# Optimization experiments

Hardware: AMD Instinct MI355X
Metric: run time of the kernel (lower is better)

Reference implementation:

```python
import jax, jax.numpy as jnp
import numpy as np


def _l2norm(t, axis=-1, eps=1e-12):
    # matches torch F.normalize: x / max(||x||, eps)
    n = jnp.sqrt(jnp.sum(t * t, axis=axis, keepdims=True))
    return t / jnp.maximum(n, eps)


def setup_inputs() -> dict:
    key = jax.random.key(0)
    ks = jax.random.split(key, 5)
    B, N, C, H = 16, 4096, 768, 12
    x = jax.random.normal(ks[0], (B, N, C), dtype=jnp.float32)
    Wqkv = jax.random.normal(ks[1], (C, 3 * C), dtype=jnp.float32) * (C ** -0.5)
    bqkv = jax.random.normal(ks[2], (3 * C,), dtype=jnp.float32) * 0.02
    Wproj = jax.random.normal(ks[3], (C, C), dtype=jnp.float32) * (C ** -0.5)
    bproj = jax.random.normal(ks[4], (C,), dtype=jnp.float32) * 0.02
    temperature = jnp.ones((H, 1, 1), dtype=jnp.float32)
    return {"x": x, "Wqkv": Wqkv, "bqkv": bqkv, "Wproj": Wproj,
            "bproj": bproj, "temperature": temperature}


def reference(x, Wqkv, bqkv, Wproj, bproj, temperature):
    B, N, C = x.shape
    H = temperature.shape[0]
    Dh = C // H
    qkv = x @ Wqkv + bqkv                      # [B,N,3C]
    qkv = qkv.reshape(B, N, 3, H, Dh)
    # -> [3,B,H,Dh,N] (channels-as-tokens layout)
    qkv = jnp.transpose(qkv, (2, 0, 3, 4, 1))
    q, k, v = qkv[0], qkv[1], qkv[2]           # each [B,H,Dh,N]
    q = _l2norm(q, axis=-1)
    k = _l2norm(k, axis=-1)
    # cross-covariance over channels: [B,H,Dh,Dh]
    attn = jnp.einsum('bhdn,bhen->bhde', q, k) * temperature
    attn = jax.nn.softmax(attn, axis=-1)
    out = jnp.einsum('bhde,bhen->bhdn', attn, v)  # [B,H,Dh,N]
    out = jnp.transpose(out, (0, 3, 1, 2)).reshape(B, N, C)
    return out @ Wproj + bproj
```

## Files before the change

### kernel.cpp

```cpp
#include <hip/hip_runtime.h>

typedef __bf16 bf16x8 __attribute__((ext_vector_type(8)));
typedef float  f32x4  __attribute__((ext_vector_type(4)));
typedef unsigned short u16x8 __attribute__((ext_vector_type(8)));
typedef unsigned short u16x4 __attribute__((ext_vector_type(4)));

#define MFMA16(a, b, c) __builtin_amdgcn_mfma_f32_16x16x32_bf16((a), (b), (c), 0, 0, 0)

#define GLOAD16(g, l) __builtin_amdgcn_global_load_lds( \
    (const __attribute__((address_space(1))) void*)(g),  \
    (__attribute__((address_space(3))) void*)(l), 16, 0, 0)

__device__ __forceinline__ float bf2f(unsigned short u) {
    unsigned int x = ((unsigned int)u) << 16;
    return __builtin_bit_cast(float, x);
}
__device__ __forceinline__ unsigned short f2bf(float f) {
    unsigned int x = __builtin_bit_cast(unsigned int, f);
    x = x + 0x7FFFu + ((x >> 16) & 1u);
    return (unsigned short)(x >> 16);
}
__device__ __forceinline__ bool is_f32(const unsigned short* tf) { return tf[0] == 0; }
__device__ __forceinline__ float ldscal(const void* p, int i, bool f32m) {
    return f32m ? ((const float*)p)[i] : bf2f(((const unsigned short*)p)[i]);
}

__global__ __launch_bounds__(256)
void conv_x(const void* __restrict__ in, unsigned short* __restrict__ out,
            const unsigned short* __restrict__ tf)
{
    const bool f32m = is_f32(tf);
    const int n8 = 6291456;
    for (int i = blockIdx.x * 256 + threadIdx.x; i < n8; i += gridDim.x * 256) {
        u16x8 v;
        if (f32m) {
            const float* p = (const float*)in + (size_t)i * 8;
            f32x4 a = *(const f32x4*)p;
            f32x4 b = *(const f32x4*)(p + 4);
#pragma unroll
            for (int j = 0; j < 4; ++j) { v[j] = f2bf(a[j]); v[4 + j] = f2bf(b[j]); }
        } else {
            v = *(const u16x8*)((const unsigned short*)in + (size_t)i * 8);
        }
        *(u16x8*)&out[(size_t)i * 8] = v;
    }
}

__global__ __launch_bounds__(256)
void tr_conv(const void* __restrict__ in_, unsigned short* __restrict__ out,
             int R, int C, int istride, const unsigned short* __restrict__ tf)
{
    __shared__ unsigned short T[64 * 72];
    const bool f32m = is_f32(tf);
    const int nct = C >> 6;
    const int tx = blockIdx.x % nct;
    const int ty = blockIdx.x / nct;
    const int r0 = ty * 64, c0 = tx * 64;
    const int t = threadIdx.x;
#pragma unroll
    for (int s = 0; s < 2; ++s) {
        const int idx = t + s * 256;
        const int rr = idx >> 3;
        const int cc = (idx & 7) * 8;
        unsigned short v[8];
        if (f32m) {
            const float* inf = (const float*)in_;
            f32x4 a = *(const f32x4*)&inf[(size_t)(r0 + rr) * istride + c0 + cc];
            f32x4 b = *(const f32x4*)&inf[(size_t)(r0 + rr) * istride + c0 + cc + 4];
#pragma unroll
            for (int j = 0; j < 4; ++j) { v[j] = f2bf(a[j]); v[4 + j] = f2bf(b[j]); }
        } else {
            u16x8 a = *(const u16x8*)&((const unsigned short*)in_)[(size_t)(r0 + rr) * istride + c0 + cc];
#pragma unroll
            for (int j = 0; j < 8; ++j) v[j] = a[j];
        }
#pragma unroll
        for (int j = 0; j < 8; ++j) T[(cc + j) * 72 + rr] = v[j];
    }
    __syncthreads();
#pragma unroll
    for (int s = 0; s < 2; ++s) {
        const int idx = t + s * 256;
        const int cc = idx >> 3;
        const int rr = (idx & 7) * 8;
        u16x8 v = *(const u16x8*)&T[cc * 72 + rr];
        *(u16x8*)&out[(size_t)(c0 + cc) * R + r0 + rr] = v;
    }
}

__global__ __launch_bounds__(256)
void conv_wv(const void* __restrict__ Wqkv, unsigned short* __restrict__ Wv_bf,
             const unsigned short* __restrict__ tf)
{
    const bool f32m = is_f32(tf);
    const int t = blockIdx.x * 256 + threadIdx.x;
    const int c = t / 96;
    const int e0 = (t % 96) * 8;
    u16x8 v;
    if (f32m) {
        const float* p = (const float*)Wqkv + (size_t)c * 2304 + 1536 + e0;
        f32x4 a = *(const f32x4*)p;
        f32x4 b = *(const f32x4*)(p + 4);
#pragma unroll
        for (int j = 0; j < 4; ++j) { v[j] = f2bf(a[j]); v[4 + j] = f2bf(b[j]); }
    } else {
        v = *(const u16x8*)&((const unsigned short*)Wqkv)[(size_t)c * 2304 + 1536 + e0];
    }
    *(u16x8*)&Wv_bf[(size_t)c * 768 + e0] = v;
}

template<int MODE>
__global__ __launch_bounds__(512, 2)
void gemm256(const unsigned short* __restrict__ A,
             const unsigned short* __restrict__ BT,
             const void* __restrict__ bias,
             unsigned short* __restrict__ o0,
             unsigned short* __restrict__ o1,
             float* __restrict__ oF,
             const unsigned short* __restrict__ tf)
{
    constexpr int K = 768, NT = 12;
    constexpr int NB = (MODE == 0) ? 6 : 3;
    constexpr int LDSSZ = (MODE == 0) ? 135168 : 131072;
    __shared__ __align__(16) char SM[LDSSZ];
    unsigned short* lds = (unsigned short*)SM;

    const bool f32m = is_f32(tf);
    const int tid  = threadIdx.x;
    const int wave = tid >> 6;
    const int lane = tid & 63;
    const int wm   = wave >> 2;
    const int wn   = wave & 3;
    const int lr   = lane & 15;
    const int lq   = lane >> 4;

    const int per = gridDim.x >> 3;
    const int wg  = (blockIdx.x & 7) * per + (blockIdx.x >> 3);
    const int mt  = wg / NB;
    const int nt  = wg % NB;
    const size_t m0 = (size_t)mt * 256;
    const int n0 = nt * 256;

    const unsigned short* Bt = BT + ((MODE == 1) ? ((m0 >> 12) * (size_t)589824) : (size_t)0);

    f32x4 zero = {0.f, 0.f, 0.f, 0.f};
    f32x4 acc[8][4];
#pragma unroll
    for (int i = 0; i < 8; ++i)
#pragma unroll
        for (int j = 0; j < 4; ++j) acc[i][j] = zero;

    auto STAGE = [&](int t) {
        unsigned short* la = lds + (t & 1) * 32768;
        unsigned short* lb = la + 16384;
        const unsigned short* ga = A  + m0 * K + t * 64;
        const unsigned short* gb = Bt + (size_t)n0 * K + t * 64;
#pragma unroll
        for (int it = 0; it < 4; ++it) {
            const int c = it * 512 + tid;
            const int row = c >> 3;
            const int gs = (c & 7) ^ (row & 7);
            GLOAD16(ga + (size_t)row * K + gs * 8, la + c * 8);
        }
#pragma unroll
        for (int it = 0; it < 4; ++it) {
            const int c = it * 512 + tid;
            const int row = c >> 3;
            const int gs = (c & 7) ^ (row & 7);
            GLOAD16(gb + (size_t)row * K + gs * 8, lb + c * 8);
        }
    };

    STAGE(0);
    STAGE(1);

    for (int t = 0; t < NT; ++t) {
        if (t + 1 < NT) asm volatile("s_waitcnt vmcnt(8)" ::: "memory");
        else            asm volatile("s_waitcnt vmcnt(0)" ::: "memory");
        __builtin_amdgcn_s_barrier();
        __builtin_amdgcn_sched_barrier(0);

        const char* la = (const char*)(lds + (t & 1) * 32768);
        const char* lb = la + 32768;

        bf16x8 bfr[4][2];
#pragma unroll
        for (int ni = 0; ni < 4; ++ni)
#pragma unroll
            for (int ks = 0; ks < 2; ++ks) {
                const int row = wn * 64 + ni * 16 + lr;
                const int s   = ks * 4 + lq;
                bfr[ni][ks] = *(const bf16x8*)(lb + row * 128 + ((s ^ (row & 7)) << 4));
            }
#pragma unroll
        for (int mh = 0; mh < 2; ++mh) {
            bf16x8 af[4][2];
#pragma unroll
            for (int mi = 0; mi < 4; ++mi)
#pragma unroll
                for (int ks = 0; ks < 2; ++ks) {
                    const int row = wm * 128 + mh * 64 + mi * 16 + lr;
                    const int s   = ks * 4 + lq;
                    af[mi][ks] = *(const bf16x8*)(la + row * 128 + ((s ^ (row & 7)) << 4));
                }
            __builtin_amdgcn_s_setprio(1);
#pragma unroll
            for (int mi = 0; mi < 4; ++mi)
#pragma unroll
                for (int ni = 0; ni < 4; ++ni)
#pragma unroll
                    for (int ks = 0; ks < 2; ++ks)
                        acc[mh * 4 + mi][ni] = MFMA16(af[mi][ks], bfr[ni][ks], acc[mh * 4 + mi][ni]);
            __builtin_amdgcn_s_setprio(0);
        }

        __builtin_amdgcn_sched_barrier(0);
        __builtin_amdgcn_s_barrier();
        if (t + 2 < NT) STAGE(t + 2);
    }

    float bb[4];
#pragma unroll
    for (int ni = 0; ni < 4; ++ni) {
        const int col = n0 + wn * 64 + ni * 16 + lr;
        if (MODE == 0)      bb[ni] = ldscal(bias, col, f32m);
        else if (MODE == 1) bb[ni] = ((const float*)bias)[(m0 >> 12) * 768 + col];
        else                bb[ni] = 0.f;
    }

    if (MODE == 1 || MODE == 2) {
#pragma unroll
        for (int mi = 0; mi < 8; ++mi)
#pragma unroll
            for (int ni = 0; ni < 4; ++ni)
#pragma unroll
                for (int r = 0; r < 4; ++r) {
                    const size_t row = m0 + (size_t)(wm * 128 + mi * 16 + lq * 4 + r);
                    const int col = n0 + wn * 64 + ni * 16 + lr;
                    const float val = acc[mi][ni][r] + bb[ni];
                    if (MODE == 2)      o0[row * 768 + col] = f2bf(val);
                    else if (f32m)      oF[row * 768 + col] = val;
                    else                o0[row * 768 + col] = f2bf(val);
                }
    } else {
        unsigned short* CTw = (unsigned short*)SM + wave * (64 * 132);
        const int cbase = (n0 < 768) ? n0 : (n0 - 768);
        unsigned short* dst = (n0 < 768) ? o0 : o1;
        const int h = (cbase >> 6) + wn;
        const size_t bh = (m0 >> 12) * 12 + h;
        const int tokbase = (int)(m0 & 4095) + wm * 128;
#pragma unroll
        for (int mi = 0; mi < 8; ++mi)
#pragma unroll
            for (int ni = 0; ni < 4; ++ni) {
                u16x4 pk;
#pragma unroll
                for (int r = 0; r < 4; ++r) pk[r] = f2bf(acc[mi][ni][r] + bb[ni]);
                *(u16x4*)&CTw[(ni * 16 + lr) * 132 + mi * 16 + lq * 4] = pk;
            }
#pragma unroll
        for (int rep = 0; rep < 16; ++rep) {
            const int d = rep * 4 + lq;
            u16x8 v = *(const u16x8*)&CTw[d * 132 + lr * 8];
            *(u16x8*)&dst[(bh * 64 + d) * 4096 + tokbase + lr * 8] = v;
        }
    }
}

__global__ __launch_bounds__(256)
void attn_sm(const unsigned short* __restrict__ qt,
             const unsigned short* __restrict__ ktb,
             const unsigned short* __restrict__ tf,
             unsigned short* __restrict__ attnT)
{
    __shared__ float S[64][64];
    __shared__ float nq[64];
    __shared__ float nk[64];
    const bool f32m = is_f32(tf);
    const int bh = blockIdx.x;
    const int h = bh % 12;
    const unsigned short* Q  = qt  + (size_t)bh * (64 * 4096);
    const unsigned short* Kp = ktb + (size_t)bh * (64 * 4096);
    const int tid = threadIdx.x;
    const int wave = tid >> 6;
    const int lane = tid & 63;
    if (tid < 64) { nq[tid] = 0.f; nk[tid] = 0.f; }

    f32x4 zero = {0.f, 0.f, 0.f, 0.f};
    f32x4 acc[4][4];
#pragma unroll
    for (int i = 0; i < 4; ++i)
#pragma unroll
        for (int j = 0; j < 4; ++j) acc[i][j] = zero;
    float sq[4] = {0.f, 0.f, 0.f, 0.f};
    float sk[4] = {0.f, 0.f, 0.f, 0.f};

    const int lr = lane & 15;
    const int lk = (lane >> 4) * 8;

    for (int it = 0; it < 32; ++it) {
        const int nb = (it * 4 + wave) * 32 + lk;
        u16x8 qa[4], ka[4];
#pragma unroll
        for (int mi = 0; mi < 4; ++mi)
            qa[mi] = *(const u16x8*)&Q[(size_t)(mi * 16 + lr) * 4096 + nb];
#pragma unroll
        for (int ni = 0; ni < 4; ++ni)
            ka[ni] = *(const u16x8*)&Kp[(size_t)(ni * 16 + lr) * 4096 + nb];
#pragma unroll
        for (int mi = 0; mi < 4; ++mi)
#pragma unroll
            for (int j = 0; j < 8; ++j) { float f = bf2f(qa[mi][j]); sq[mi] += f * f; }
#pragma unroll
        for (int ni = 0; ni < 4; ++ni)
#pragma unroll
            for (int j = 0; j < 8; ++j) { float f = bf2f(ka[ni][j]); sk[ni] += f * f; }
#pragma unroll
        for (int mi = 0; mi < 4; ++mi)
#pragma unroll
            for (int ni = 0; ni < 4; ++ni)
                acc[mi][ni] = MFMA16(__builtin_bit_cast(bf16x8, qa[mi]),
                                     __builtin_bit_cast(bf16x8, ka[ni]),
                                     acc[mi][ni]);
    }

    for (int ww = 0; ww < 4; ++ww) {
        if (wave == ww) {
#pragma unroll
            for (int mi = 0; mi < 4; ++mi)
#pragma unroll
                for (int ni = 0; ni < 4; ++ni)
#pragma unroll
                    for (int r = 0; r < 4; ++r) {
                        const int d = mi * 16 + (lane >> 4) * 4 + r;
                        const int e = ni * 16 + lr;
                        if (ww == 0) S[d][e] = acc[mi][ni][r];
                        else         S[d][e] += acc[mi][ni][r];
                    }
        }
        __syncthreads();
    }

#pragma unroll
    for (int mi = 0; mi < 4; ++mi) {
        float v = sq[mi];
        v += __shfl_xor(v, 16); v += __shfl_xor(v, 32);
        if (lane < 16) atomicAdd(&nq[mi * 16 + lane], v);
        float v2 = sk[mi];
        v2 += __shfl_xor(v2, 16); v2 += __shfl_xor(v2, 32);
        if (lane < 16) atomicAdd(&nk[mi * 16 + lane], v2);
    }
    __syncthreads();

    const int d  = tid >> 2;
    const int qq = tid & 3;
    const float tv = f32m ? ((const float*)tf)[h] : bf2f(tf[h]);
    const float qn = fmaxf(sqrtf(nq[d]), 1e-12f);
    float vals[16];
    float mx = -1e30f;
#pragma unroll
    for (int i = 0; i < 16; ++i) {
        const int e = qq * 16 + i;
        const float s = S[d][e] / (qn * fmaxf(sqrtf(nk[e]), 1e-12f)) * tv;
        vals[i] = s;
        mx = fmaxf(mx, s);
    }
    mx = fmaxf(mx, __shfl_xor(mx, 1));
    mx = fmaxf(mx, __shfl_xor(mx, 2));
    float sum = 0.f;
#pragma unroll
    for (int i = 0; i < 16; ++i) { vals[i] = __expf(vals[i] - mx); sum += vals[i]; }
    sum += __shfl_xor(sum, 1);
    sum += __shfl_xor(sum, 2);
    const float inv = 1.0f / sum;
#pragma unroll
    for (int i = 0; i < 16; ++i) {
        const int e = qq * 16 + i;
        attnT[(size_t)bh * 4096 + e * 64 + d] = f2bf(vals[i] * inv);
    }
}

__global__ __launch_bounds__(512)
void mb_build(const unsigned short* __restrict__ attnT,
              const unsigned short* __restrict__ WprojT,
              unsigned short* __restrict__ MbT)
{
    const int bh = blockIdx.x;
    const int b = bh / 12, h = bh % 12;
    const int tid = threadIdx.x;
    const int wave = tid >> 6;
    const int lane = tid & 63;
    const unsigned short* At = attnT + (size_t)bh * 4096;

    f32x4 zero = {0.f, 0.f, 0.f, 0.f};
    f32x4 acc[4][6];
#pragma unroll
    for (int i = 0; i < 4; ++i)
#pragma unroll
        for (int j = 0; j < 6; ++j) acc[i][j] = zero;

    const int lr  = lane & 15;
    const int lk8 = (lane >> 4) * 8;

#pragma unroll
    for (int ks = 0; ks < 2; ++ks) {
        bf16x8 af[4], bfr[6];
#pragma unroll
        for (int mi = 0; mi < 4; ++mi)
            af[mi] = *(const bf16x8*)&At[(mi * 16 + lr) * 64 + ks * 32 + lk8];
#pragma unroll
        for (int ni = 0; ni < 6; ++ni) {
            const int j = wave * 96 + ni * 16 + lr;
            bfr[ni] = *(const bf16x8*)&WprojT[(size_t)j * 768 + h * 64 + ks * 32 + lk8];
        }
#pragma unroll
        for (int mi = 0; mi < 4; ++mi)
#pragma unroll
            for (int ni = 0; ni < 6; ++ni)
                acc[mi][ni] = MFMA16(af[mi], bfr[ni], acc[mi][ni]);
    }

#pragma unroll
    for (int mi = 0; mi < 4; ++mi)
#pragma unroll
        for (int ni = 0; ni < 6; ++ni) {
            const int e = mi * 16 + (lane >> 4) * 4;
            const int j = wave * 96 + ni * 16 + lr;
            u16x4 pk;
#pragma unroll
            for (int r = 0; r < 4; ++r) pk[r] = f2bf(acc[mi][ni][r]);
            *(u16x4*)&MbT[(size_t)b * 589824 + (size_t)j * 768 + h * 64 + e] = pk;
        }
}

__global__ __launch_bounds__(256)
void beff_k(const unsigned short* __restrict__ MbT,
            const void* __restrict__ bqkv, const void* __restrict__ bp,
            float* __restrict__ beff, const unsigned short* __restrict__ tf)
{
    __shared__ float bv[768];
    const bool f32m = is_f32(tf);
    for (int i = threadIdx.x; i < 768; i += 256) bv[i] = ldscal(bqkv, 1536 + i, f32m);
    __syncthreads();
    const int t = blockIdx.x * 256 + threadIdx.x;
    const int b = t / 768, j = t % 768;
    float s = ldscal(bp, j, f32m);
    const unsigned short* row = MbT + (size_t)b * 589824 + (size_t)j * 768;
    for (int e8 = 0; e8 < 96; ++e8) {
        u16x8 m = *(const u16x8*)&row[e8 * 8];
#pragma unroll
        for (int jj = 0; jj < 8; ++jj) s += bf2f(m[jj]) * bv[e8 * 8 + jj];
    }
    beff[t] = s;
}

extern "C" void kernel_launch(void* const* d_in, const int* in_sizes, int n_in,
                              void* d_out, int out_size, void* d_ws, size_t ws_size,
                              hipStream_t stream)
{
    const void* x    = d_in[0];
    const void* Wqkv = d_in[1];
    const void* bqkv = d_in[2];
    const void* Wp   = d_in[3];
    const void* bp   = d_in[4];
    const unsigned short* tf = (const unsigned short*)d_in[5];

    char* w = (char*)d_ws;
    unsigned short* qt     = (unsigned short*)(w);
    unsigned short* PT     = (unsigned short*)(w);
    float*          beff   = (float*)(w + 18874368);
    unsigned short* ktb    = (unsigned short*)(w + 100663296);
    unsigned short* xb     = (unsigned short*)(w + 201326592);
    unsigned short* WqkT   = (unsigned short*)(w + 301989888);
    unsigned short* Wv_bf  = (unsigned short*)(w + 304349184);
    unsigned short* attnT  = (unsigned short*)(w + 305528832);
    unsigned short* MbT    = (unsigned short*)(w + 307101696);
    unsigned short* WprojT = (unsigned short*)(w + 325976064);

    conv_x <<<dim3(2048), dim3(256), 0, stream>>>(x, xb, tf);
    tr_conv<<<dim3(288),  dim3(256), 0, stream>>>(Wqkv, WqkT, 768, 1536, 2304, tf);
    conv_wv<<<dim3(288),  dim3(256), 0, stream>>>(Wqkv, Wv_bf, tf);
    tr_conv<<<dim3(144),  dim3(256), 0, stream>>>(Wp, WprojT, 768, 768, 768, tf);

    gemm256<0><<<dim3(1536), dim3(512), 0, stream>>>(xb, WqkT, bqkv, qt, ktb, nullptr, tf);
    attn_sm<<<dim3(192), dim3(256), 0, stream>>>(qt, ktb, tf, attnT);
    mb_build<<<dim3(192), dim3(512), 0, stream>>>(attnT, WprojT, MbT);
    gemm256<2><<<dim3(144), dim3(512), 0, stream>>>(MbT, Wv_bf, nullptr, PT, nullptr, nullptr, tf);
    beff_k<<<dim3(48), dim3(256), 0, stream>>>(MbT, bqkv, bp, beff, tf);
    gemm256<1><<<dim3(768), dim3(512), 0, stream>>>(xb, PT, beff,
        (unsigned short*)d_out, nullptr, (float*)d_out, tf);
}
```

Before: 488.1 us.

## Split GEMM k-tile into four barrier-synchronized phases with smaller fragments

The GEMM main loop now splits each 64-wide k-tile into four phases. Each phase reads one k-slice of A and B fragments from LDS into half-size register arrays and runs one quarter of the MFMAs, with workgroup barriers between phases. The next tile's global-to-LDS prefetch is issued before the final MFMA quarter so load issue overlaps compute. Holding fewer fragments lowers register pressure, at the cost of extra barriers and lgkmcnt waits per iteration. The LDS base pointer is now computed from `SM` rather than `lds`.

Result: no change. 494.9 us (+1.4%).

```diff
diff --git a/kernel.cpp b/kernel.cpp
--- a/kernel.cpp
+++ b/kernel.cpp
@@ -151,8 +151,8 @@
         for (int j = 0; j < 4; ++j) acc[i][j] = zero;
 
     auto STAGE = [&](int t) {
-        unsigned short* la = lds + (t & 1) * 32768;
-        unsigned short* lb = la + 16384;
+        unsigned short* la_ = lds + (t & 1) * 32768;
+        unsigned short* lb_ = la_ + 16384;
         const unsigned short* ga = A  + m0 * K + t * 64;
         const unsigned short* gb = Bt + (size_t)n0 * K + t * 64;
 #pragma unroll
@@ -160,64 +160,75 @@
             const int c = it * 512 + tid;
             const int row = c >> 3;
             const int gs = (c & 7) ^ (row & 7);
-            GLOAD16(ga + (size_t)row * K + gs * 8, la + c * 8);
+            GLOAD16(ga + (size_t)row * K + gs * 8, la_ + c * 8);
         }
 #pragma unroll
         for (int it = 0; it < 4; ++it) {
             const int c = it * 512 + tid;
             const int row = c >> 3;
             const int gs = (c & 7) ^ (row & 7);
-            GLOAD16(gb + (size_t)row * K + gs * 8, lb + c * 8);
+            GLOAD16(gb + (size_t)row * K + gs * 8, lb_ + c * 8);
         }
     };
 
     STAGE(0);
     STAGE(1);
 
+    bf16x8 af[4], bfr[4];
+
+#define READ_B(ks) do { \
+    _Pragma("unroll") for (int ni = 0; ni < 4; ++ni) { \
+        const int row = wn * 64 + ni * 16 + lr; \
+        bfr[ni] = *(const bf16x8*)(lb + row * 128 + ((((ks) * 4 + lq) ^ (row & 7)) << 4)); } } while (0)
+#define READ_A(mh, ks) do { \
+    _Pragma("unroll") for (int mi = 0; mi < 4; ++mi) { \
+        const int row = wm * 128 + (mh) * 64 + mi * 16 + lr; \
+        af[mi] = *(const bf16x8*)(la + row * 128 + ((((ks) * 4 + lq) ^ (row & 7)) << 4)); } } while (0)
+#define MFMA_Q(mh) do { \
+    _Pragma("unroll") for (int mi = 0; mi < 4; ++mi) \
+    _Pragma("unroll") for (int ni = 0; ni < 4; ++ni) \
+        acc[(mh) * 4 + mi][ni] = MFMA16(af[mi], bfr[ni], acc[(mh) * 4 + mi][ni]); } while (0)
+#define PH_MID() do { \
+    __builtin_amdgcn_sched_barrier(0); \
+    __builtin_amdgcn_s_barrier(); \
+    asm volatile("s_waitcnt lgkmcnt(0)" ::: "memory"); \
+    __builtin_amdgcn_sched_barrier(0); } while (0)
+#define PH_END() do { \
+    __builtin_amdgcn_sched_barrier(0); \
+    __builtin_amdgcn_s_barrier(); } while (0)
+
     for (int t = 0; t < NT; ++t) {
-        if (t + 1 < NT) asm volatile("s_waitcnt vmcnt(8)" ::: "memory");
+        if (t < NT - 1) asm volatile("s_waitcnt vmcnt(8)" ::: "memory");
         else            asm volatile("s_waitcnt vmcnt(0)" ::: "memory");
         __builtin_amdgcn_s_barrier();
-        __builtin_amdgcn_sched_barrier(0);
-
-        const char* la = (const char*)(lds + (t & 1) * 32768);
+
+        const char* la = (const char*)SM + (t & 1) * 65536;
         const char* lb = la + 32768;
 
-        bf16x8 bfr[4][2];
-#pragma unroll
-        for (int ni = 0; ni < 4; ++ni)
-#pragma unroll
-            for (int ks = 0; ks < 2; ++ks) {
-                const int row = wn * 64 + ni * 16 + lr;
-                const int s   = ks * 4 + lq;
-                bfr[ni][ks] = *(const bf16x8*)(lb + row * 128 + ((s ^ (row & 7)) << 4));
-            }
-#pragma unroll
-        for (int mh = 0; mh < 2; ++mh) {
-            bf16x8 af[4][2];
-#pragma unroll
-            for (int mi = 0; mi < 4; ++mi)
-#pragma unroll
-                for (int ks = 0; ks < 2; ++ks) {
-                    const int row = wm * 128 + mh * 64 + mi * 16 + lr;
-                    const int s   = ks * 4 + lq;
-                    af[mi][ks] = *(const bf16x8*)(la + row * 128 + ((s ^ (row & 7)) << 4));
-                }
-            __builtin_amdgcn_s_setprio(1);
-#pragma unroll
-            for (int mi = 0; mi < 4; ++mi)
-#pragma unroll
-                for (int ni = 0; ni < 4; ++ni)
-#pragma unroll
-                    for (int ks = 0; ks < 2; ++ks)
-                        acc[mh * 4 + mi][ni] = MFMA16(af[mi][ks], bfr[ni][ks], acc[mh * 4 + mi][ni]);
-            __builtin_amdgcn_s_setprio(0);
-        }
-
+        READ_B(0); READ_A(0, 0);
+        PH_MID();
+        __builtin_amdgcn_s_setprio(1); MFMA_Q(0); __builtin_amdgcn_s_setprio(0);
+        PH_END();
+        READ_A(1, 0);
+        PH_MID();
+        __builtin_amdgcn_s_setprio(1); MFMA_Q(1); __builtin_amdgcn_s_setprio(0);
+        PH_END();
+        READ_B(1); READ_A(0, 1);
+        PH_MID();
+        __builtin_amdgcn_s_setprio(1); MFMA_Q(0); __builtin_amdgcn_s_setprio(0);
+        PH_END();
+        READ_A(1, 1);
+        asm volatile("s_waitcnt lgkmcnt(0)" ::: "memory");
         __builtin_amdgcn_sched_barrier(0);
         __builtin_amdgcn_s_barrier();
         if (t + 2 < NT) STAGE(t + 2);
-    }
+        __builtin_amdgcn_s_setprio(1); MFMA_Q(1); __builtin_amdgcn_s_setprio(0);
+    }
+#undef READ_B
+#undef READ_A
+#undef MFMA_Q
+#undef PH_MID
+#undef PH_END
 
     float bb[4];
 #pragma unroll
```
